# Kernel optimization log

Measured on AMD Instinct MI355X. Metric: run time of the kernel, lower is better.

## Reference

```python
import jax, jax.numpy as jnp
import numpy as np
import math

B, S, DK, DV = 8, 2048, 128, 128
SQRT_DK = math.sqrt(DK)


def setup_inputs() -> dict:
    key = jax.random.key(0)
    kq, kk, kv = jax.random.split(key, 3)
    Q = jax.random.normal(kq, (B, S, DK), dtype=jnp.float32)
    K = jax.random.normal(kk, (B, S, DK), dtype=jnp.float32)
    V = jax.random.normal(kv, (B, S, DV), dtype=jnp.float32)
    # additive causal mask, broadcast over batch: 0 on/below diag, -1e9 above
    causal = jnp.tril(jnp.ones((S, S), dtype=bool))
    mask = jnp.where(causal, 0.0, -1e9).astype(jnp.float32)[None]  # [1, S, S]
    return {"Q": Q, "K": K, "V": V, "mask": mask}


def reference(Q, K, V, mask):
    # QK = Q @ K^T / sqrt(dk); dropout is identity in eval mode.
    scores = jnp.einsum("bqd,bkd->bqk", Q, K) / SQRT_DK + mask  # [B, S, S]
    # transpose->softmax(dim=1)->transpose == softmax over key axis (last dim)
    A = jax.nn.softmax(scores, axis=-1)
    return jnp.einsum("bqk,bkv->bqv", A, V)  # [B, S, DV]
```

## Files before the change

kernel.cpp:

```cpp
#include <hip/hip_runtime.h>

#define SEQ 2048
#define DHEAD 128
#define NB 8
#define KST 136
#define VST 72
#define PST 72
#define PR 1792

typedef short short8 __attribute__((ext_vector_type(8)));
typedef float f32x4 __attribute__((ext_vector_type(4)));

__device__ __constant__ unsigned char UNIT[72] = {
    120,121,122,123,124,125,126,127,
    112,113,114,115,116,117,118,
    104,105,106,107,108,109,110,
    96,97,98,99,100,101,
    88,89,90,91,92,93,
    80,81,82,83,84,
    72,73,74,75,76,
    64,65,66,67,
    56,57,58,59,
    48,49,50,
    40,41,42,
    32,33,
    24,25,
    16,
    8,
    119,102,85,68,51,34,17,0
};

__device__ __forceinline__ unsigned short f2bf(float x) {
    unsigned int u = __float_as_uint(x);
    u += 0x7fffu + ((u >> 16) & 1u);
    return (unsigned short)(u >> 16);
}

__device__ __forceinline__ float bf2f(unsigned short h) {
    return __uint_as_float(((unsigned int)h) << 16);
}

__global__ void prep(const float* __restrict__ K, const float* __restrict__ V,
                     unsigned short* __restrict__ Kb, unsigned short* __restrict__ Vt) {
    if (blockIdx.x < 2048) {
        int i = blockIdx.x * 256 + threadIdx.x;
        float4 v = ((const float4*)K)[i];
        ushort4 o;
        o.x = f2bf(v.x); o.y = f2bf(v.y); o.z = f2bf(v.z); o.w = f2bf(v.w);
        ((ushort4*)Kb)[i] = o;
    } else {
        __shared__ unsigned short t[32][33];
        int bx = blockIdx.x - 2048;
        int b = bx >> 8, xy = bx & 255;
        int s0 = (xy >> 2) << 5;
        int d0 = (xy & 3) << 5;
        int tid = threadIdx.x;
        int sl = tid >> 3, dl = (tid & 7) << 2;
        float4 v = *(const float4*)&V[(b * SEQ + s0 + sl) * DHEAD + d0 + dl];
        t[sl][dl + 0] = f2bf(v.x); t[sl][dl + 1] = f2bf(v.y);
        t[sl][dl + 2] = f2bf(v.z); t[sl][dl + 3] = f2bf(v.w);
        __syncthreads();
        int dr = tid >> 3, sr = (tid & 7) << 2;
        ushort4 o;
        o.x = t[sr + 0][dr]; o.y = t[sr + 1][dr]; o.z = t[sr + 2][dr]; o.w = t[sr + 3][dr];
        *(ushort4*)&Vt[(b * DHEAD + d0 + dr) * SEQ + s0 + sr] = o;
    }
}

__global__ __launch_bounds__(256, 2)
void flash_attn(const float* __restrict__ Q, const unsigned short* __restrict__ Kb,
                const unsigned short* __restrict__ Vt,
                unsigned short* __restrict__ Opart, float* __restrict__ lsumP,
                float* __restrict__ out) {
    __shared__ __align__(16) unsigned short Klds[64 * KST];
    __shared__ __align__(16) unsigned short Vlds[128 * VST];
    __shared__ __align__(16) unsigned short Pb[4][32 * PST];

    const int b = blockIdx.x & 7;
    const int e = UNIT[blockIdx.x >> 3];
    const int qt = e >> 3, c = e & 7;
    const int kt0 = c * 4;
    const int kt1 = min(2 * qt + 2, kt0 + 4);

    const int tid = threadIdx.x;
    const int w = tid >> 6, lane = tid & 63;
    const int ln15 = lane & 15, g = lane >> 4;
    const int qrow0 = qt * 128 + w * 32;

    const float scale = 0.08838834764831845f;
    short8 qf[2][4];
#pragma unroll
    for (int nt = 0; nt < 2; ++nt) {
        const float* qp = Q + (b * SEQ + qrow0 + nt * 16 + ln15) * DHEAD + g * 8;
#pragma unroll
        for (int cc = 0; cc < 4; ++cc) {
            float4 a = *(const float4*)(qp + cc * 32);
            float4 d = *(const float4*)(qp + cc * 32 + 4);
            short8 f;
            f[0] = f2bf(a.x * scale); f[1] = f2bf(a.y * scale);
            f[2] = f2bf(a.z * scale); f[3] = f2bf(a.w * scale);
            f[4] = f2bf(d.x * scale); f[5] = f2bf(d.y * scale);
            f[6] = f2bf(d.z * scale); f[7] = f2bf(d.w * scale);
            qf[nt][cc] = f;
        }
    }

    f32x4 acc[2][8];
#pragma unroll
    for (int nt = 0; nt < 2; ++nt)
#pragma unroll
        for (int j = 0; j < 8; ++j) acc[nt][j] = (f32x4){0.f, 0.f, 0.f, 0.f};
    float lsum[2] = {0.f, 0.f};
    unsigned short* P = &Pb[w][0];

    {
        const int k0 = kt0 << 6;
        short8 pre[8];
#pragma unroll
        for (int j = 0; j < 4; ++j) {
            int ck = tid + j * 256;
            pre[j]     = *(const short8*)(Kb + (b * SEQ + k0 + (ck >> 4)) * DHEAD + (ck & 15) * 8);
            pre[4 + j] = *(const short8*)(Vt + (b * DHEAD + (ck >> 3)) * SEQ + k0 + (ck & 7) * 8);
        }
#pragma unroll
        for (int j = 0; j < 4; ++j) {
            int ck = tid + j * 256;
            *(short8*)&Klds[(ck >> 4) * KST + (ck & 15) * 8] = pre[j];
            *(short8*)&Vlds[(ck >> 3) * VST + (ck & 7) * 8]  = pre[4 + j];
        }
    }
    __syncthreads();

    for (int kt = kt0; kt < kt1; ++kt) {
        const int k0 = kt << 6;
        const bool have_next = (kt + 1 < kt1);
        short8 pre2[8];
        if (have_next) {
            const int kn = (kt + 1) << 6;
#pragma unroll
            for (int j = 0; j < 4; ++j) {
                int ck = tid + j * 256;
                pre2[j]     = *(const short8*)(Kb + (b * SEQ + kn + (ck >> 4)) * DHEAD + (ck & 15) * 8);
                pre2[4 + j] = *(const short8*)(Vt + (b * DHEAD + (ck >> 3)) * SEQ + kn + (ck & 7) * 8);
            }
        }

        if (k0 <= qrow0 + 31) {
            const bool nm = (k0 + 63 > qrow0);
#pragma unroll
            for (int mtp = 0; mtp < 2; ++mtp) {
                short8 kf[8];
#pragma unroll
                for (int cc = 0; cc < 4; ++cc) {
                    kf[cc]     = *(const short8*)&Klds[((2 * mtp) * 16 + ln15) * KST + cc * 32 + g * 8];
                    kf[4 + cc] = *(const short8*)&Klds[((2 * mtp + 1) * 16 + ln15) * KST + cc * 32 + g * 8];
                }
                f32x4 s00 = (f32x4){0.f, 0.f, 0.f, 0.f};
                f32x4 s01 = (f32x4){0.f, 0.f, 0.f, 0.f};
                f32x4 s10 = (f32x4){0.f, 0.f, 0.f, 0.f};
                f32x4 s11 = (f32x4){0.f, 0.f, 0.f, 0.f};
#pragma unroll
                for (int cc = 0; cc < 4; ++cc) {
                    s00 = __builtin_amdgcn_mfma_f32_16x16x32_bf16(kf[cc],     qf[0][cc], s00, 0, 0, 0);
                    s10 = __builtin_amdgcn_mfma_f32_16x16x32_bf16(kf[4 + cc], qf[0][cc], s10, 0, 0, 0);
                    s01 = __builtin_amdgcn_mfma_f32_16x16x32_bf16(kf[cc],     qf[1][cc], s01, 0, 0, 0);
                    s11 = __builtin_amdgcn_mfma_f32_16x16x32_bf16(kf[4 + cc], qf[1][cc], s11, 0, 0, 0);
                }
#pragma unroll
                for (int h = 0; h < 2; ++h) {
#pragma unroll
                    for (int nt = 0; nt < 2; ++nt) {
                        f32x4 s = h ? (nt ? s11 : s10) : (nt ? s01 : s00);
                        const int mt = 2 * mtp + h;
                        float p[4];
#pragma unroll
                        for (int r = 0; r < 4; ++r) {
                            p[r] = __expf(s[r]);
                            if (nm) {
                                int colg = k0 + mt * 16 + g * 4 + r;
                                int rowg = qrow0 + nt * 16 + ln15;
                                p[r] = (colg <= rowg) ? p[r] : 0.f;
                            }
                        }
                        lsum[nt] += (p[0] + p[1]) + (p[2] + p[3]);
                        uint2 dd;
                        dd.x = __builtin_amdgcn_perm(__float_as_uint(p[1]), __float_as_uint(p[0]), 0x07060302u);
                        dd.y = __builtin_amdgcn_perm(__float_as_uint(p[3]), __float_as_uint(p[2]), 0x07060302u);
                        *(uint2*)&P[(nt * 16 + ln15) * PST + mt * 16 + g * 4] = dd;
                    }
                }
            }
#pragma unroll
            for (int c2 = 0; c2 < 2; ++c2) {
                short8 vf[8];
#pragma unroll
                for (int nt2 = 0; nt2 < 8; ++nt2)
                    vf[nt2] = *(const short8*)&Vlds[(nt2 * 16 + ln15) * VST + c2 * 32 + g * 8];
#pragma unroll
                for (int nt = 0; nt < 2; ++nt) {
                    short8 pf = *(const short8*)&P[(nt * 16 + ln15) * PST + c2 * 32 + g * 8];
#pragma unroll
                    for (int nt2 = 0; nt2 < 8; ++nt2)
                        acc[nt][nt2] = __builtin_amdgcn_mfma_f32_16x16x32_bf16(pf, vf[nt2], acc[nt][nt2], 0, 0, 0);
                }
            }
        }

        if (have_next) {
            __syncthreads();
#pragma unroll
            for (int j = 0; j < 4; ++j) {
                int ck = tid + j * 256;
                *(short8*)&Klds[(ck >> 4) * KST + (ck & 15) * 8] = pre2[j];
                *(short8*)&Vlds[(ck >> 3) * VST + (ck & 7) * 8]  = pre2[4 + j];
            }
            __syncthreads();
        }
    }

#pragma unroll
    for (int nt = 0; nt < 2; ++nt) {
        float v = lsum[nt];
        v += __shfl_xor(v, 16);
        v += __shfl_xor(v, 32);
        lsum[nt] = v;
    }

    if (qt < 2) {
#pragma unroll
        for (int nt = 0; nt < 2; ++nt) {
            float inv[4];
#pragma unroll
            for (int r = 0; r < 4; ++r) inv[r] = 1.0f / __shfl(lsum[nt], g * 4 + r);
#pragma unroll
            for (int nt2 = 0; nt2 < 8; ++nt2) {
#pragma unroll
                for (int r = 0; r < 4; ++r) {
                    int rowg = qrow0 + nt * 16 + g * 4 + r;
                    out[(b * SEQ + rowg) * DHEAD + nt2 * 16 + ln15] = acc[nt][nt2][r] * inv[r];
                }
            }
        }
    } else {
#pragma unroll
        for (int nt = 0; nt < 2; ++nt)
            if (lane < 16)
                lsumP[(c * NB + b) * PR + qrow0 + nt * 16 + lane - 256] = lsum[nt];
#pragma unroll
        for (int nt = 0; nt < 2; ++nt) {
#pragma unroll
            for (int nt2 = 0; nt2 < 8; ++nt2) {
#pragma unroll
                for (int r = 0; r < 4; ++r) {
                    int r2 = qrow0 + nt * 16 + g * 4 + r - 256;
                    Opart[((c * NB + b) * PR + r2) * DHEAD + nt2 * 16 + ln15] = f2bf(acc[nt][nt2][r]);
                }
            }
        }
    }
}

__global__ void finalize(const unsigned short* __restrict__ Opart,
                         const float* __restrict__ lsumP, float* __restrict__ out) {
    int b = blockIdx.y;
    int gx = blockIdx.x * 256 + threadIdx.x;
    int d4 = gx & 31;
    int r2 = gx >> 5;
    int row = 256 + r2;
    int nch = (row >> 8) + 1;
    float4 o = {0.f, 0.f, 0.f, 0.f};
    float l = 0.f;
    for (int cc = 0; cc < nch; ++cc) {
        ushort4 ph = ((const ushort4*)Opart)[((cc * NB + b) * PR + r2) * 32 + d4];
        o.x += bf2f(ph.x); o.y += bf2f(ph.y); o.z += bf2f(ph.z); o.w += bf2f(ph.w);
        l += lsumP[(cc * NB + b) * PR + r2];
    }
    float inv = 1.0f / l;
    float4 r;
    r.x = o.x * inv; r.y = o.y * inv; r.z = o.z * inv; r.w = o.w * inv;
    ((float4*)out)[(b * SEQ + row) * 32 + d4] = r;
}

extern "C" void kernel_launch(void* const* d_in, const int* in_sizes, int n_in,
                              void* d_out, int out_size, void* d_ws, size_t ws_size,
                              hipStream_t stream) {
    const float* Q = (const float*)d_in[0];
    const float* K = (const float*)d_in[1];
    const float* V = (const float*)d_in[2];
    float* out = (float*)d_out;

    const int NE = NB * SEQ * DHEAD;
    unsigned short* Kb = (unsigned short*)d_ws;
    unsigned short* Vt = Kb + NE;
    unsigned short* Opart = Vt + NE;
    float* lsumP = (float*)(Opart + 8 * NB * PR * DHEAD);

    prep<<<4096, 256, 0, stream>>>(K, V, Kb, Vt);
    flash_attn<<<576, 256, 0, stream>>>(Q, Kb, Vt, Opart, lsumP, out);
    finalize<<<dim3(224, NB), 256, 0, stream>>>(Opart, lsumP, out);
}
```

Measured before the change: 111.3 us.

## Fuse K/V bf16 conversion and V transpose into attention tile loads

Removes the separate prep kernel that converted K and V to bf16 and wrote a transposed V to workspace. The attention kernel now loads fp32 K and V tiles directly, packs pairs to bf16 with a perm instruction, and writes V transposed into LDS. This drops one launch and a full write/read round trip of the converted tensors. In exchange it doubles global bytes per tile load, adds more prefetch registers that may pressure occupancy, and repeats conversion work across blocks that share K/V tiles.

```diff
diff --git a/kernel.cpp b/kernel.cpp
--- a/kernel.cpp
+++ b/kernel.cpp
@@ -40,36 +40,16 @@
     return __uint_as_float(((unsigned int)h) << 16);
 }
 
-__global__ void prep(const float* __restrict__ K, const float* __restrict__ V,
-                     unsigned short* __restrict__ Kb, unsigned short* __restrict__ Vt) {
-    if (blockIdx.x < 2048) {
-        int i = blockIdx.x * 256 + threadIdx.x;
-        float4 v = ((const float4*)K)[i];
-        ushort4 o;
-        o.x = f2bf(v.x); o.y = f2bf(v.y); o.z = f2bf(v.z); o.w = f2bf(v.w);
-        ((ushort4*)Kb)[i] = o;
-    } else {
-        __shared__ unsigned short t[32][33];
-        int bx = blockIdx.x - 2048;
-        int b = bx >> 8, xy = bx & 255;
-        int s0 = (xy >> 2) << 5;
-        int d0 = (xy & 3) << 5;
-        int tid = threadIdx.x;
-        int sl = tid >> 3, dl = (tid & 7) << 2;
-        float4 v = *(const float4*)&V[(b * SEQ + s0 + sl) * DHEAD + d0 + dl];
-        t[sl][dl + 0] = f2bf(v.x); t[sl][dl + 1] = f2bf(v.y);
-        t[sl][dl + 2] = f2bf(v.z); t[sl][dl + 3] = f2bf(v.w);
-        __syncthreads();
-        int dr = tid >> 3, sr = (tid & 7) << 2;
-        ushort4 o;
-        o.x = t[sr + 0][dr]; o.y = t[sr + 1][dr]; o.z = t[sr + 2][dr]; o.w = t[sr + 3][dr];
-        *(ushort4*)&Vt[(b * DHEAD + d0 + dr) * SEQ + s0 + sr] = o;
-    }
+__device__ __forceinline__ unsigned int pack2bf(float lo, float hi) {
+    unsigned int ul = __float_as_uint(lo), uh = __float_as_uint(hi);
+    ul += 0x7fffu + ((ul >> 16) & 1u);
+    uh += 0x7fffu + ((uh >> 16) & 1u);
+    return __builtin_amdgcn_perm(uh, ul, 0x07060302u);
 }
 
 __global__ __launch_bounds__(256, 2)
-void flash_attn(const float* __restrict__ Q, const unsigned short* __restrict__ Kb,
-                const unsigned short* __restrict__ Vt,
+void flash_attn(const float* __restrict__ Q, const float* __restrict__ K,
+                const float* __restrict__ V,
                 unsigned short* __restrict__ Opart, float* __restrict__ lsumP,
                 float* __restrict__ out) {
     __shared__ __align__(16) unsigned short Klds[64 * KST];
@@ -86,6 +66,8 @@
     const int w = tid >> 6, lane = tid & 63;
     const int ln15 = lane & 15, g = lane >> 4;
     const int qrow0 = qt * 128 + w * 32;
+
+    const int sp = tid & 31, dgp = tid >> 5;
 
     const float scale = 0.08838834764831845f;
     short8 qf[2][4];
@@ -115,18 +97,33 @@
 
     {
         const int k0 = kt0 << 6;
-        short8 pre[8];
+        float4 kx[8], va[4], vb[4];
+        const float* Kp = K + (b * SEQ + k0) * DHEAD;
+#pragma unroll
+        for (int j = 0; j < 8; ++j) {
+            int idx = tid + j * 256;
+            kx[j] = *(const float4*)(Kp + (idx >> 5) * DHEAD + (idx & 31) * 4);
+        }
+        const float* Vp = V + (b * SEQ + k0 + 2 * sp) * DHEAD + 16 * dgp;
 #pragma unroll
         for (int j = 0; j < 4; ++j) {
-            int ck = tid + j * 256;
-            pre[j]     = *(const short8*)(Kb + (b * SEQ + k0 + (ck >> 4)) * DHEAD + (ck & 15) * 8);
-            pre[4 + j] = *(const short8*)(Vt + (b * DHEAD + (ck >> 3)) * SEQ + k0 + (ck & 7) * 8);
+            va[j] = *(const float4*)(Vp + 4 * j);
+            vb[j] = *(const float4*)(Vp + DHEAD + 4 * j);
+        }
+#pragma unroll
+        for (int j = 0; j < 8; ++j) {
+            int idx = tid + j * 256;
+            uint2 p;
+            p.x = pack2bf(kx[j].x, kx[j].y);
+            p.y = pack2bf(kx[j].z, kx[j].w);
+            *(uint2*)&Klds[(idx >> 5) * KST + (idx & 31) * 4] = p;
         }
 #pragma unroll
         for (int j = 0; j < 4; ++j) {
-            int ck = tid + j * 256;
-            *(short8*)&Klds[(ck >> 4) * KST + (ck & 15) * 8] = pre[j];
-            *(short8*)&Vlds[(ck >> 3) * VST + (ck & 7) * 8]  = pre[4 + j];
+            *(unsigned int*)&Vlds[(16 * dgp + 4 * j + 0) * VST + 2 * sp] = pack2bf(va[j].x, vb[j].x);
+            *(unsigned int*)&Vlds[(16 * dgp + 4 * j + 1) * VST + 2 * sp] = pack2bf(va[j].y, vb[j].y);
+            *(unsigned int*)&Vlds[(16 * dgp + 4 * j + 2) * VST + 2 * sp] = pack2bf(va[j].z, vb[j].z);
+            *(unsigned int*)&Vlds[(16 * dgp + 4 * j + 3) * VST + 2 * sp] = pack2bf(va[j].w, vb[j].w);
         }
     }
     __syncthreads();
@@ -134,14 +131,20 @@
     for (int kt = kt0; kt < kt1; ++kt) {
         const int k0 = kt << 6;
         const bool have_next = (kt + 1 < kt1);
-        short8 pre2[8];
+        float4 kx2[8], va2[4], vb2[4];
         if (have_next) {
             const int kn = (kt + 1) << 6;
+            const float* Kp = K + (b * SEQ + kn) * DHEAD;
+#pragma unroll
+            for (int j = 0; j < 8; ++j) {
+                int idx = tid + j * 256;
+                kx2[j] = *(const float4*)(Kp + (idx >> 5) * DHEAD + (idx & 31) * 4);
+            }
+            const float* Vp = V + (b * SEQ + kn + 2 * sp) * DHEAD + 16 * dgp;
 #pragma unroll
             for (int j = 0; j < 4; ++j) {
-                int ck = tid + j * 256;
-                pre2[j]     = *(const short8*)(Kb + (b * SEQ + kn + (ck >> 4)) * DHEAD + (ck & 15) * 8);
-                pre2[4 + j] = *(const short8*)(Vt + (b * DHEAD + (ck >> 3)) * SEQ + kn + (ck & 7) * 8);
+                va2[j] = *(const float4*)(Vp + 4 * j);
+                vb2[j] = *(const float4*)(Vp + DHEAD + 4 * j);
             }
         }
 
@@ -209,10 +212,19 @@
         if (have_next) {
             __syncthreads();
 #pragma unroll
+            for (int j = 0; j < 8; ++j) {
+                int idx = tid + j * 256;
+                uint2 p;
+                p.x = pack2bf(kx2[j].x, kx2[j].y);
+                p.y = pack2bf(kx2[j].z, kx2[j].w);
+                *(uint2*)&Klds[(idx >> 5) * KST + (idx & 31) * 4] = p;
+            }
+#pragma unroll
             for (int j = 0; j < 4; ++j) {
-                int ck = tid + j * 256;
-                *(short8*)&Klds[(ck >> 4) * KST + (ck & 15) * 8] = pre2[j];
-                *(short8*)&Vlds[(ck >> 3) * VST + (ck & 7) * 8]  = pre2[4 + j];
+                *(unsigned int*)&Vlds[(16 * dgp + 4 * j + 0) * VST + 2 * sp] = pack2bf(va2[j].x, vb2[j].x);
+                *(unsigned int*)&Vlds[(16 * dgp + 4 * j + 1) * VST + 2 * sp] = pack2bf(va2[j].y, vb2[j].y);
+                *(unsigned int*)&Vlds[(16 * dgp + 4 * j + 2) * VST + 2 * sp] = pack2bf(va2[j].z, vb2[j].z);
+                *(unsigned int*)&Vlds[(16 * dgp + 4 * j + 3) * VST + 2 * sp] = pack2bf(va2[j].w, vb2[j].w);
             }
             __syncthreads();
         }
@@ -289,13 +301,9 @@
     const float* V = (const float*)d_in[2];
     float* out = (float*)d_out;
 
-    const int NE = NB * SEQ * DHEAD;
-    unsigned short* Kb = (unsigned short*)d_ws;
-    unsigned short* Vt = Kb + NE;
-    unsigned short* Opart = Vt + NE;
+    unsigned short* Opart = (unsigned short*)d_ws;
     float* lsumP = (float*)(Opart + 8 * NB * PR * DHEAD);
 
-    prep<<<4096, 256, 0, stream>>>(K, V, Kb, Vt);
-    flash_attn<<<576, 256, 0, stream>>>(Q, Kb, Vt, Opart, lsumP, out);
+    flash_attn<<<576, 256, 0, stream>>>(Q, K, V, Opart, lsumP, out);
     finalize<<<dim3(224, NB), 256, 0, stream>>>(Opart, lsumP, out);
 }
```

Result: no change. 112.9 us (+1.4%).
